# Optimization experiments

Measured on AMD Instinct MI355X. Metric: run time of the kernel, lower is better.

The kernel has to match this reference:

```python
import jax, jax.numpy as jnp
import numpy as np

NUM_GRAPHS = 1024
EPS = 1e-5  # BatchNorm eps
NEG_SLOPE = 0.2  # GATConv leaky_relu slope


def _bn(x, g, b):
    # train-mode BatchNorm over node/graph axis (biased variance, as torch)
    mu = jnp.mean(x, axis=0)
    var = jnp.mean((x - mu) ** 2, axis=0)
    return (x - mu) * jax.lax.rsqrt(var + EPS) * g + b


def _prelu(x, a):
    return jnp.where(x > 0, x, a * x)


def _gat_layer(x, src, dst, W, a_src, a_dst, bias, n_nodes):
    # single-head GATConv (heads=1, concat=True), self-loops already in src/dst
    h = x @ W                                            # [N, C]
    e = jax.nn.leaky_relu(jnp.take(h @ a_src, src) + jnp.take(h @ a_dst, dst), NEG_SLOPE)  # [E]
    m = jax.ops.segment_max(e, dst, num_segments=n_nodes)
    ex = jnp.exp(e - jnp.take(m, dst))
    denom = jax.ops.segment_sum(ex, dst, num_segments=n_nodes)
    alpha = ex / (jnp.take(denom, dst) + 1e-16)          # softmax over in-edges of each target
    out = jax.ops.segment_sum(jnp.take(h, src, axis=0) * alpha[:, None], dst, num_segments=n_nodes)
    return out + bias


def setup_inputs() -> dict:
    key = jax.random.key(0)
    ks = jax.random.split(key, 16)
    N, E, F, H, C = 500_000, 8_000_000, 7, 8, 2

    def gl(k, shp, fan_in):
        return (jax.random.normal(k, shp, jnp.float32) / np.sqrt(fan_in)).astype(jnp.float32)

    return {
        "x": jax.random.normal(ks[0], (N, F), jnp.float32),
        "edge_index": jax.random.randint(ks[1], (2, E), 0, N, jnp.int32),
        "batch": jnp.sort(jax.random.randint(ks[2], (N,), 0, NUM_GRAPHS, jnp.int32)),
        "W1": gl(ks[3], (F, H), F), "as1": gl(ks[4], (H,), H), "ad1": gl(ks[5], (H,), H), "b1": jnp.zeros((H,), jnp.float32),
        "W2": gl(ks[6], (H, H), H), "as2": gl(ks[7], (H,), H), "ad2": gl(ks[8], (H,), H), "b2": jnp.zeros((H,), jnp.float32),
        "W3": gl(ks[9], (H, H), H), "as3": gl(ks[10], (H,), H), "ad3": gl(ks[11], (H,), H), "b3": jnp.zeros((H,), jnp.float32),
        "g1": jnp.ones((H,), jnp.float32), "be1": jnp.zeros((H,), jnp.float32),
        "g2": jnp.ones((H,), jnp.float32), "be2": jnp.zeros((H,), jnp.float32),
        "g3": jnp.ones((H,), jnp.float32), "be3": jnp.zeros((H,), jnp.float32),
        "a_gnn": jnp.float32(0.25),
        "Wjk": gl(ks[12], (3 * H, H), 3 * H), "bjk": jnp.zeros((H,), jnp.float32),
        "Wm1": gl(ks[13], (H, H), H), "bm1": jnp.zeros((H,), jnp.float32),
        "gm": jnp.ones((H,), jnp.float32), "bem": jnp.zeros((H,), jnp.float32),
        "a_mlp": jnp.float32(0.25),
        "Wm2": gl(ks[14], (H, C), H), "bm2": jnp.zeros((C,), jnp.float32),
    }


def reference(x, edge_index, batch,
              W1, as1, ad1, b1, W2, as2, ad2, b2, W3, as3, ad3, b3,
              g1, be1, g2, be2, g3, be3, a_gnn, Wjk, bjk,
              Wm1, bm1, gm, bem, a_mlp, Wm2, bm2):
    N = x.shape[0]
    loop = jnp.arange(N, dtype=edge_index.dtype)  # GATConv add_self_loops=True
    src = jnp.concatenate([edge_index[0], loop])
    dst = jnp.concatenate([edge_index[1], loop])
    # 3-layer GAT, each: conv -> BatchNorm -> PReLU (dropout omitted: eval)
    h1 = _prelu(_bn(_gat_layer(x, src, dst, W1, as1, ad1, b1, N), g1, be1), a_gnn)
    h2 = _prelu(_bn(_gat_layer(h1, src, dst, W2, as2, ad2, b2, N), g2, be2), a_gnn)
    h3 = _prelu(_bn(_gat_layer(h2, src, dst, W3, as3, ad3, b3, N), g3, be3), a_gnn)
    # JumpingKnowledge 'cat' + projection to out_channels
    h = jnp.concatenate([h1, h2, h3], axis=1) @ Wjk + bjk   # [N, 8]
    pooled = jax.ops.segment_sum(h, batch, num_segments=NUM_GRAPHS)  # global_add_pool [G, 8]
    m1 = _prelu(_bn(pooled @ Wm1 + bm1, gm, bem), a_mlp)    # MLP hidden
    return m1 @ Wm2 + bm2                                    # [G, 2] logits
```

## Files before the change

kernel.cpp:

```cpp
#include <hip/hip_runtime.h>

typedef unsigned short u16;
typedef unsigned int   u32;

#define EPSBN     1e-5f
#define NEG_SLOPE 0.2f
#define NGRAPH    1024
#define NPB       512
#define CHUNK     16384
#define BKCAP     11264
#define NTILE     8
#define SLOTS     1536


static __device__ __forceinline__ float bfl(const u16* __restrict__ p, int i){
    return __uint_as_float(((u32)p[i]) << 16);
}
static __device__ __forceinline__ float ldf(const void* __restrict__ p, int i, bool f32){
    return f32 ? ((const float*)p)[i] : bfl((const u16*)p, i);
}
static __device__ __forceinline__ u16 f2bf(float f){
    u32 u = __float_as_uint(f);
    return (u16)((u + 0x7fffu + ((u >> 16) & 1u)) >> 16);
}
static __device__ __forceinline__ void unpack8(uint4 pk, float* a){
    a[0] = __uint_as_float((pk.x & 0xffffu) << 16);
    a[1] = __uint_as_float( pk.x & 0xffff0000u);
    a[2] = __uint_as_float((pk.y & 0xffffu) << 16);
    a[3] = __uint_as_float( pk.y & 0xffff0000u);
    a[4] = __uint_as_float((pk.z & 0xffffu) << 16);
    a[5] = __uint_as_float( pk.z & 0xffff0000u);
    a[6] = __uint_as_float((pk.w & 0xffffu) << 16);
    a[7] = __uint_as_float( pk.w & 0xffff0000u);
}
static __device__ __forceinline__ uint4 pack8(const float* a){
    uint4 pk;
    pk.x = (u32)f2bf(a[0]) | ((u32)f2bf(a[1])<<16);
    pk.y = (u32)f2bf(a[2]) | ((u32)f2bf(a[3])<<16);
    pk.z = (u32)f2bf(a[4]) | ((u32)f2bf(a[5])<<16);
    pk.w = (u32)f2bf(a[6]) | ((u32)f2bf(a[7])<<16);
    return pk;
}

static __device__ __forceinline__ int wave_scan_incl(int x){
    int lane = threadIdx.x & 63;
    #pragma unroll
    for (int off = 1; off < 64; off <<= 1){
        int y = __shfl_up(x, off, 64);
        if (lane >= off) x += y;
    }
    return x;
}
static __device__ __forceinline__ int block_scan_incl(int x, int* wpart){
    int t = threadIdx.x, lane = t & 63, wv = t >> 6;
    int nw = blockDim.x >> 6;
    int ws = wave_scan_incl(x);
    __syncthreads();
    if (lane == 63) wpart[wv] = ws;
    __syncthreads();
    if (wv == 0){
        int p = (lane < nw) ? wpart[lane] : 0;
        p = wave_scan_incl(p);
        if (lane < nw) wpart[lane] = p;
    }
    __syncthreads();
    int base = wv ? wpart[wv-1] : 0;
    return base + ws;
}

__global__ __launch_bounds__(1024) void k_binsort(const int* __restrict__ src,
                                                  const int* __restrict__ dst,
                                                  u32* __restrict__ stage,
                                                  int* __restrict__ matL,
                                                  int E, int B,
                                                  const u16* __restrict__ x16,
                                                  int* __restrict__ dflag,
                                                  float* __restrict__ statsAll){
    __shared__ u32 pr[CHUNK];
    __shared__ int h[2048];
    __shared__ int wpart[16];
    int c = blockIdx.x, t = threadIdx.x;
    if (c == 0){
        if (t < 64){
            bool hit = false;
            for (int i = t; i < 128; i += 64){
                float v = bfl(x16, i);
                if (!(fabsf(v) <= 1e6f)) hit = true;
            }
            unsigned long long m = __ballot(hit);
            if (t == 0) dflag[0] = (m != 0ull) ? 1 : 0;
        }
        if (t >= 64 && t < 112) statsAll[t - 64] = 0.f;
    }
    int e0 = c << 14, e1 = min(e0 + CHUNK, E), cn = e1 - e0;
    for (int b = t; b < B; b += 1024) h[b] = 0;
    __syncthreads();
    for (int i = e0 + t; i < e1; i += 1024) atomicAdd(&h[dst[i] >> 9], 1);
    __syncthreads();
    int base = t << 1, run = 0, loc[2];
    #pragma unroll
    for (int j = 0; j < 2; j++){
        int b = base + j;
        int v = (b < B) ? h[b] : 0;
        loc[j] = run; run += v;
    }
    int incl = block_scan_incl(run, wpart);
    int bex = incl - run;
    __syncthreads();
    #pragma unroll
    for (int j = 0; j < 2; j++){
        int b = base + j;
        if (b < B) h[b] = bex + loc[j];
    }
    __syncthreads();
    int* mrow = matL + (size_t)c * (B+1);
    for (int b = t; b < B; b += 1024) mrow[b] = h[b];
    if (t == 0) mrow[B] = cn;
    __syncthreads();
    for (int i = e0 + t; i < e1; i += 1024){
        int d = dst[i];
        int b = d >> 9;
        int p = atomicAdd(&h[b], 1);
        pr[p] = ((u32)src[i] << 9) | (u32)(d & 511);
    }
    __syncthreads();
    u32* srow = stage + ((size_t)c << 14);
    for (int i = t; i < cn; i += 1024) srow[i] = pr[i];
}

__global__ __launch_bounds__(1024) void k_bucket(const u32* __restrict__ stage,
                                                 const int* __restrict__ matL,
                                                 int* __restrict__ tileOfs,
                                                 u32* __restrict__ csr,
                                                 int N, int B, int NC){
    __shared__ u32 pr[BKCAP];
    __shared__ int hist[4096];
    __shared__ int sc[1024];
    __shared__ int lofsA[512];
    __shared__ int wpart[16];
    int k = blockIdx.x, t = threadIdx.x;
    int n0 = k << 9, n1 = min(n0 + NPB, N), nn = n1 - n0;
    int cnt = 0, lofs = 0;
    if (t < NC){
        lofs = matL[(size_t)t*(B+1) + k];
        cnt  = matL[(size_t)t*(B+1) + k + 1] - lofs;
    }
    if (t < 512) lofsA[t] = lofs;
    int incl1 = block_scan_incl(cnt, wpart);
    sc[t] = incl1;
    __syncthreads();
    int total = sc[1023];
    int ec    = min(total, BKCAP - nn);
    for (int pidx = t; pidx < ec; pidx += 1024){
        int lo = 0, hi = 511;
        while (lo < hi){ int mid = (lo + hi) >> 1; if (sc[mid] > pidx) hi = mid; else lo = mid + 1; }
        int segStart = lo ? sc[lo-1] : 0;
        pr[pidx] = stage[((size_t)lo << 14) + lofsA[lo] + (pidx - segStart)];
    }
    __syncthreads();
    for (int j = t; j < nn; j += 1024) pr[ec + j] = ((u32)(n0 + j) << 9) | (u32)j;
    int ecnt = ec + nn;
    for (int i = t; i < 4096; i += 1024) hist[i] = 0;
    __syncthreads();
    for (int i = t; i < ecnt; i += 1024){
        u32 pk = pr[i];
        int dl = pk & 511;
        int tile = min((int)(pk >> 9) >> 16, NTILE-1);
        atomicAdd(&hist[(tile << 9) + dl], 1);
    }
    __syncthreads();
    int base = t << 2, run = 0, loc[4];
    #pragma unroll
    for (int j = 0; j < 4; j++){ loc[j] = run; run += hist[base + j]; }
    int incl2 = block_scan_incl(run, wpart);
    int bex = incl2 - run;
    __syncthreads();
    #pragma unroll
    for (int j = 0; j < 4; j++) hist[base + j] = bex + loc[j];
    if ((t & 127) == 0) tileOfs[(size_t)k*9 + (t >> 7)] = bex;
    if (t == 0)         tileOfs[(size_t)k*9 + 8] = ecnt;
    __syncthreads();
    size_t wbase = (size_t)k * BKCAP;
    for (int i = t; i < ecnt; i += 1024){
        u32 pk = pr[i];
        int dl = pk & 511;
        int tile = min((int)(pk >> 9) >> 16, NTILE-1);
        int p = atomicAdd(&hist[(tile << 9) + dl], 1);
        csr[wbase + p] = pk;
    }
}

__global__ void k_transform(const uint4* __restrict__ actpk, const void* __restrict__ xraw,
                            const int* __restrict__ dflag, int fin,
                            const void* __restrict__ W, const void* __restrict__ adst,
                            const float* __restrict__ stats, const void* __restrict__ gamma,
                            const void* __restrict__ beta, const void* __restrict__ alpha,
                            uint4* __restrict__ hrec, float* __restrict__ hd, int n){
    const bool f32 = dflag[0] != 0;
    __shared__ float Wl[64], dl[8], scl[8], sft[8], alv;
    int t = threadIdx.x;
    if (t < 64)            Wl[t]   = (t < fin*8) ? ldf(W, t, f32) : 0.f;
    if (t >= 64 && t < 72) dl[t-64] = ldf(adst, t-64, f32);
    if (t == 80) alv = ldf(alpha, 0, f32);
    if (stats && t < 8){
        float invN = 1.f/(float)n;
        float mu  = stats[t]*invN;
        float var = fmaxf(stats[8+t]*invN - mu*mu, 0.f);
        float s   = ldf(gamma, t, f32)*rsqrtf(var + EPSBN);
        scl[t] = s; sft[t] = ldf(beta, t, f32) - mu*s;
    }
    __syncthreads();
    int i = blockIdx.x*blockDim.x + t;
    if (i >= n) return;
    float a[8];
    if (xraw){
        #pragma unroll
        for (int k=0;k<7;k++) a[k] = ldf(xraw, i*7 + k, f32);
        a[7] = 0.f;
    } else {
        unpack8(actpk[i], a);
        #pragma unroll
        for (int j=0;j<8;j++){
            float y = a[j]*scl[j] + sft[j];
            a[j] = (y > 0.f) ? y : alv*y;
        }
    }
    float h[8];
    #pragma unroll
    for (int j=0;j<8;j++){
        float acc = 0.f;
        #pragma unroll
        for (int k=0;k<8;k++) acc += a[k]*Wl[k*8+j];
        h[j] = acc;
    }
    float s2 = 0.f;
    #pragma unroll
    for (int j=0;j<8;j++) s2 += h[j]*dl[j];
    hd[i] = s2;
    hrec[i] = pack8(h);
}

__global__ __launch_bounds__(512) void k_aggregate(
        const u32* __restrict__ csr,
        const int* __restrict__ tileOfs,
        const uint4* __restrict__ hrec, const float* __restrict__ hd,
        const void* __restrict__ asrc, const int* __restrict__ dflag,
        uint4* __restrict__ act, float* __restrict__ stats, int n){
    const bool f32 = dflag[0] != 0;
    __shared__ u32   stg[4*SLOTS];
    __shared__ float swp[SLOTS];
    __shared__ u16   sdl[SLOTS];
    __shared__ float hdl[512];
    __shared__ u16 bs[512], be[512];
    __shared__ float alS[8];
    __shared__ float sred[8][16];
    __shared__ int tofS[9];
    int k = blockIdx.x, t = threadIdx.x;
    int n0 = k << 9;
    int nn = min(NPB, n - n0);
    if (t < 8) alS[t] = ldf(asrc, t, f32);
    if (t < 9) tofS[t] = tileOfs[(size_t)k*9 + t];
    hdl[t] = (t < nn) ? hd[n0 + t] : 0.f;
    const u32* ecsr = csr + (size_t)k * BKCAP;
    __syncthreads();
    float al[8];
    #pragma unroll
    for (int j = 0; j < 8; j++) al[j] = alS[j];
    float acc[8] = {0,0,0,0,0,0,0,0};
    float den = 0.f;

    int wt = 0, wc = 0;
    while (wt < NTILE && wc >= tofS[wt+1]){ wt++; if (wt < NTILE) wc = tofS[wt]; }

    u32 pkc[3]; uint4 hvc[3];
    if (wt < NTILE){
        int L = min(SLOTS, tofS[wt+1] - wc);
        #pragma unroll
        for (int j = 0; j < 3; j++) pkc[j] = ecsr[wc + min(t + (j << 9), L - 1)];
        #pragma unroll
        for (int j = 0; j < 3; j++) hvc[j] = hrec[pkc[j] >> 9];
    }

    while (wt < NTILE){
        int L = min(SLOTS, tofS[wt+1] - wc);
        __syncthreads();
        #pragma unroll
        for (int j = 0; j < 3; j++){
            int i = t + (j << 9);
            float h[8]; unpack8(hvc[j], h);
            int dl = (int)(pkc[j] & 511u);
            float e = hdl[dl];
            #pragma unroll
            for (int q = 0; q < 8; q++) e += h[q]*al[q];
            e = (e > 0.f) ? e : NEG_SLOPE*e;
            float w = __expf(e);
            if (i < L){
                stg[0*SLOTS + i] = hvc[j].x;
                stg[1*SLOTS + i] = hvc[j].y;
                stg[2*SLOTS + i] = hvc[j].z;
                stg[3*SLOTS + i] = hvc[j].w;
                swp[i] = w;
                sdl[i] = (u16)dl;
            }
        }
        bs[t] = 0; be[t] = 0;
        __syncthreads();
        int nwt = wt, nwc = wc + SLOTS;
        while (nwt < NTILE && nwc >= tofS[nwt+1]){ nwt++; if (nwt < NTILE) nwc = tofS[nwt]; }
        if (nwt < NTILE){
            int Ln = min(SLOTS, tofS[nwt+1] - nwc);
            #pragma unroll
            for (int j = 0; j < 3; j++) pkc[j] = ecsr[nwc + min(t + (j << 9), Ln - 1)];
            #pragma unroll
            for (int j = 0; j < 3; j++) hvc[j] = hrec[pkc[j] >> 9];
        }
        for (int i = t; i < L; i += 512){
            int dl = (int)sdl[i];
            if (i == 0){
                bs[dl] = 0;
            } else {
                int dp = (int)sdl[i - 1];
                if (dp != dl){ bs[dl] = (u16)i; be[dp] = (u16)i; }
            }
            if (i == L-1) be[dl] = (u16)L;
        }
        __syncthreads();
        {
            int p0 = bs[t], p1 = be[t];
            for (int p = p0; p < p1; ++p){
                uint4 hv = make_uint4(stg[0*SLOTS + p], stg[1*SLOTS + p],
                                      stg[2*SLOTS + p], stg[3*SLOTS + p]);
                float h[8]; unpack8(hv, h);
                float w = swp[p];
                den += w;
                #pragma unroll
                for (int q = 0; q < 8; q++) acc[q] += w*h[q];
            }
        }
        wt = nwt; wc = nwc;
    }

    float o[8] = {0,0,0,0,0,0,0,0};
    if (t < nn){
        float inv = 1.f/(den + 1e-16f);
        #pragma unroll
        for (int j = 0; j < 8; j++) o[j] = acc[j]*inv;
        act[n0 + t] = pack8(o);
    }
    float v[16];
    #pragma unroll
    for (int j=0;j<8;j++){ v[j]=o[j]; v[8+j]=o[j]*o[j]; }
    #pragma unroll
    for (int off=32; off>0; off>>=1){
        #pragma unroll
        for (int j=0;j<16;j++) v[j] += __shfl_down(v[j], off, 64);
    }
    int lane = t & 63, wv = t >> 6;
    if (lane == 0){
        #pragma unroll
        for (int j=0;j<16;j++) sred[wv][j] = v[j];
    }
    __syncthreads();
    if (t < 16){
        float tot = 0.f;
        #pragma unroll
        for (int w=0; w<8; w++) tot += sred[w][t];
        atomicAdd(&stats[t], tot);
    }
}

static __device__ __forceinline__ int lowerb(const int* __restrict__ a, int n, int key){
    int lo = 0, hi = n;
    while (lo < hi){ int mid = (lo + hi) >> 1; if (a[mid] < key) lo = mid + 1; else hi = mid; }
    return lo;
}

__global__ __launch_bounds__(256) void k_jkpool(
        const uint4* __restrict__ a1, const uint4* __restrict__ a2, const uint4* __restrict__ a3,
        const float* __restrict__ st1, const float* __restrict__ st2, const float* __restrict__ st3,
        const void* __restrict__ g1, const void* __restrict__ be1,
        const void* __restrict__ g2, const void* __restrict__ be2,
        const void* __restrict__ g3, const void* __restrict__ be3,
        const void* __restrict__ alpha,
        const void* __restrict__ Wjk, const void* __restrict__ bjk,
        const int* __restrict__ dflag,
        const int* __restrict__ batch, float* __restrict__ pooled, int n){
    const bool f32 = dflag[0] != 0;
    __shared__ float Wl[192], bl[8], scl[24], sft[24], alv;
    __shared__ int rng[2];
    int t = threadIdx.x, g = blockIdx.x;
    if (t < 192) Wl[t] = ldf(Wjk, t, f32);
    if (t < 8)   bl[t] = ldf(bjk, t, f32);
    if (t < 24){
        int L = t >> 3, j = t & 7;
        const float* st = (L==0)? st1 : (L==1)? st2 : st3;
        const void* gg  = (L==0)? g1  : (L==1)? g2  : g3;
        const void* bb_ = (L==0)? be1 : (L==1)? be2 : be3;
        float invN = 1.f/(float)n;
        float mu  = st[j]*invN;
        float var = fmaxf(st[8+j]*invN - mu*mu, 0.f);
        float s   = ldf(gg, j, f32)*rsqrtf(var + EPSBN);
        scl[t] = s; sft[t] = ldf(bb_, j, f32) - mu*s;
    }
    if (t == 30) alv = ldf(alpha, 0, f32);
    if (t == 0) rng[0] = lowerb(batch, n, g);
    if (t == 1) rng[1] = lowerb(batch, n, g+1);
    __syncthreads();
    int lo = rng[0], hi = rng[1];
    float pa[8] = {0,0,0,0,0,0,0,0};
    for (int i = lo + t; i < hi; i += 256){
        float c[24];
        unpack8(a1[i], c);
        unpack8(a2[i], c+8);
        unpack8(a3[i], c+16);
        #pragma unroll
        for (int k=0;k<24;k++){
            float y = c[k]*scl[k] + sft[k];
            c[k] = (y > 0.f) ? y : alv*y;
        }
        #pragma unroll
        for (int j=0;j<8;j++){
            float acc = bl[j];
            #pragma unroll
            for (int k=0;k<24;k++) acc += c[k]*Wl[k*8+j];
            pa[j] += acc;
        }
    }
    #pragma unroll
    for (int off=32; off>0; off>>=1){
        #pragma unroll
        for (int j=0;j<8;j++) pa[j] += __shfl_down(pa[j], off, 64);
    }
    __shared__ float sr[4][8];
    int lane = t & 63, wv = t >> 6;
    if (lane == 0){
        #pragma unroll
        for (int j=0;j<8;j++) sr[wv][j] = pa[j];
    }
    __syncthreads();
    if (t < 8){
        float tot = sr[0][t]+sr[1][t]+sr[2][t]+sr[3][t];
        pooled[(size_t)g*8 + t] = tot;
    }
}

__global__ __launch_bounds__(1024) void k_final(
        const float* __restrict__ pooled,
        const void* __restrict__ Wm1, const void* __restrict__ bm1,
        const void* __restrict__ gm, const void* __restrict__ bem,
        const void* __restrict__ am,
        const void* __restrict__ Wm2, const void* __restrict__ bm2,
        const int* __restrict__ dflag,
        float* __restrict__ out, int G){
    const bool f32 = dflag[0] != 0;
    int t = threadIdx.x;
    float tv[8] = {0,0,0,0,0,0,0,0};
    if (t < G){
        float r[8];
        #pragma unroll
        for (int j=0;j<8;j++) r[j] = pooled[(size_t)t*8+j];
        #pragma unroll
        for (int j=0;j<8;j++){
            float acc = ldf(bm1, j, f32);
            #pragma unroll
            for (int k=0;k<8;k++) acc += r[k]*ldf(Wm1, k*8+j, f32);
            tv[j] = acc;
        }
    }
    float v[16];
    #pragma unroll
    for (int j=0;j<8;j++){ v[j]=tv[j]; v[8+j]=tv[j]*tv[j]; }
    #pragma unroll
    for (int off=32; off>0; off>>=1){
        #pragma unroll
        for (int j=0;j<16;j++) v[j] += __shfl_down(v[j], off, 64);
    }
    __shared__ float sred[16][16];
    int lane = t & 63, wv = t >> 6;
    if (lane == 0){
        #pragma unroll
        for (int j=0;j<16;j++) sred[wv][j] = v[j];
    }
    __syncthreads();
    __shared__ float stt[16];
    if (t < 16){
        float tot = 0.f;
        #pragma unroll
        for (int w=0; w<16; w++) tot += sred[w][t];
        stt[t] = tot;
    }
    __syncthreads();
    if (t < G){
        float a = ldf(am, 0, f32);
        float invG = 1.f/(float)G;
        float m1[8];
        #pragma unroll
        for (int j=0;j<8;j++){
            float mu  = stt[j]*invG;
            float var = fmaxf(stt[8+j]*invG - mu*mu, 0.f);
            float y = (tv[j]-mu)*rsqrtf(var+EPSBN)*ldf(gm,j,f32)+ldf(bem,j,f32);
            m1[j] = (y>0.f)? y : a*y;
        }
        #pragma unroll
        for (int c=0;c<2;c++){
            float oacc = ldf(bm2, c, f32);
            #pragma unroll
            for (int k=0;k<8;k++) oacc += m1[k]*ldf(Wm2, k*2+c, f32);
            out[(size_t)t*2+c] = oacc;
        }
    }
}

extern "C" void kernel_launch(void* const* d_in, const int* in_sizes, int n_in,
                              void* d_out, int out_size, void* d_ws, size_t ws_size,
                              hipStream_t stream){
    const u16* x16   = (const u16*)d_in[0];
    const void* x    = d_in[0];
    const int* ei    = (const int*)d_in[1];
    const int* batch = (const int*)d_in[2];
    int N = in_sizes[2];
    int E = in_sizes[1] / 2;
    const int* srcA = ei;
    const int* dstA = ei + E;
    const void *W1=d_in[3],  *as1=d_in[4],  *ad1=d_in[5];
    const void *W2=d_in[7],  *as2=d_in[8],  *ad2=d_in[9];
    const void *W3=d_in[11], *as3=d_in[12], *ad3=d_in[13];
    const void *g1=d_in[15], *be1=d_in[16];
    const void *g2=d_in[17], *be2=d_in[18];
    const void *g3=d_in[19], *be3=d_in[20];
    const void *agnn=d_in[21];
    const void *Wjk=d_in[22], *bjk=d_in[23];
    const void *Wm1=d_in[24], *bm1=d_in[25];
    const void *gm =d_in[26], *bem=d_in[27];
    const void *amlp=d_in[28];
    const void *Wm2=d_in[29], *bm2=d_in[30];

    char* p = (char*)d_ws;
    auto carve = [&](size_t bytes) -> void* {
        void* r = (void*)p;
        p += (bytes + 255) & ~(size_t)255;
        return r;
    };
    int nb512 = (N + 511)/512;
    int B  = (N + NPB - 1) / NPB;
    int NC = (E + CHUNK - 1) / CHUNK;
    int*   dflag  = (int*)  carve(256);
    int*   tileOfs= (int*)  carve((size_t)B*9*4);
    int*   matL   = (int*)  carve((size_t)NC*(B+1)*4);
    u32*   stage  = (u32*)  carve((size_t)NC*CHUNK*4);
    u32*   csr    = (u32*)  carve((size_t)B*BKCAP*4);
    uint4* hrec   = (uint4*)carve((size_t)N*16);
    float* hd     = (float*)carve((size_t)N*4);
    uint4* act1   = (uint4*)carve((size_t)N*16);
    uint4* act2   = (uint4*)carve((size_t)N*16);
    uint4* act3   = (uint4*)carve((size_t)N*16);
    float* statsA = (float*)carve(256);
    float* stats1 = statsA;
    float* stats2 = statsA + 16;
    float* stats3 = statsA + 32;
    float* pooled = (float*)carve((size_t)NGRAPH*32);
    (void)ws_size; (void)n_in;

    k_binsort <<<NC, 1024, 0, stream>>>(srcA, dstA, stage, matL, E, B, x16, dflag, statsA);
    k_bucket  <<<B, 1024, 0, stream>>>(stage, matL, tileOfs, csr, N, B, NC);

    k_transform <<<nb512, 512, 0, stream>>>(nullptr, x, dflag, 7, W1, ad1,
                                            nullptr, nullptr, nullptr, agnn, hrec, hd, N);
    k_aggregate <<<B, 512, 0, stream>>>(csr, tileOfs, hrec, hd, as1, dflag, act1, stats1, N);
    k_transform <<<nb512, 512, 0, stream>>>(act1, nullptr, dflag, 8, W2, ad2,
                                            stats1, g1, be1, agnn, hrec, hd, N);
    k_aggregate <<<B, 512, 0, stream>>>(csr, tileOfs, hrec, hd, as2, dflag, act2, stats2, N);
    k_transform <<<nb512, 512, 0, stream>>>(act2, nullptr, dflag, 8, W3, ad3,
                                            stats2, g2, be2, agnn, hrec, hd, N);
    k_aggregate <<<B, 512, 0, stream>>>(csr, tileOfs, hrec, hd, as3, dflag, act3, stats3, N);

    k_jkpool<<<NGRAPH, 256, 0, stream>>>(act1, act2, act3, stats1, stats2, stats3,
                                         g1, be1, g2, be2, g3, be3, agnn,
                                         Wjk, bjk, dflag, batch, pooled, N);
    int G = out_size / 2;
    k_final <<<1, 1024, 0, stream>>>(pooled, Wm1, bm1, gm, bem, amlp, Wm2, bm2, dflag, (float*)d_out, G);
}
```

Baseline: 514.0 us.

## Fuse layer-1 transform into bucket kernel and MLP head into pooling kernel

Moves the first GAT layer's linear transform (x@W1 and the dst attention score) into the tail of k_bucket, so one kernel launch and a pass over x are removed. It also folds the final MLP/BatchNorm head into k_jkpool, using an atomic ticket so the last block to finish computes the output, which removes the separate single-block k_final launch. The cost is extra register and shared-memory pressure in k_bucket, plus a threadfence/atomic at the end of each jkpool block.

Measured after the change: 574.3 us. 1.12x slower.

```diff
diff --git a/kernel.cpp b/kernel.cpp
--- a/kernel.cpp
+++ b/kernel.cpp
@@ -88,7 +88,7 @@
                 if (!(fabsf(v) <= 1e6f)) hit = true;
             }
             unsigned long long m = __ballot(hit);
-            if (t == 0) dflag[0] = (m != 0ull) ? 1 : 0;
+            if (t == 0){ dflag[0] = (m != 0ull) ? 1 : 0; dflag[1] = 0; }
         }
         if (t >= 64 && t < 112) statsAll[t - 64] = 0.f;
     }
@@ -132,20 +132,30 @@
                                                  const int* __restrict__ matL,
                                                  int* __restrict__ tileOfs,
                                                  u32* __restrict__ csr,
-                                                 int N, int B, int NC){
+                                                 int N, int B, int NC,
+                                                 const void* __restrict__ x,
+                                                 const void* __restrict__ W1,
+                                                 const void* __restrict__ ad1,
+                                                 const int* __restrict__ dflag,
+                                                 uint4* __restrict__ hrec,
+                                                 float* __restrict__ hd){
     __shared__ u32 pr[BKCAP];
     __shared__ int hist[4096];
     __shared__ int sc[1024];
     __shared__ int lofsA[512];
     __shared__ int wpart[16];
+    __shared__ float WlT[64], adT[8];
     int k = blockIdx.x, t = threadIdx.x;
     int n0 = k << 9, n1 = min(n0 + NPB, N), nn = n1 - n0;
+    const bool f32 = dflag[0] != 0;
     int cnt = 0, lofs = 0;
     if (t < NC){
         lofs = matL[(size_t)t*(B+1) + k];
         cnt  = matL[(size_t)t*(B+1) + k + 1] - lofs;
     }
     if (t < 512) lofsA[t] = lofs;
+    if (t >= 512 && t < 576) WlT[t-512] = ((t-512) < 56) ? ldf(W1, t-512, f32) : 0.f;
+    if (t >= 576 && t < 584) adT[t-576] = ldf(ad1, t-576, f32);
     int incl1 = block_scan_incl(cnt, wpart);
     sc[t] = incl1;
     __syncthreads();
@@ -187,6 +197,26 @@
         int tile = min((int)(pk >> 9) >> 16, NTILE-1);
         int p = atomicAdd(&hist[(tile << 9) + dl], 1);
         csr[wbase + p] = pk;
+    }
+    if (t < nn){
+        int i = n0 + t;
+        float a[8];
+        #pragma unroll
+        for (int kk = 0; kk < 7; kk++) a[kk] = ldf(x, i*7 + kk, f32);
+        a[7] = 0.f;
+        float h[8];
+        #pragma unroll
+        for (int j = 0; j < 8; j++){
+            float acc = 0.f;
+            #pragma unroll
+            for (int kk = 0; kk < 8; kk++) acc += a[kk]*WlT[kk*8+j];
+            h[j] = acc;
+        }
+        float s2 = 0.f;
+        #pragma unroll
+        for (int j = 0; j < 8; j++) s2 += h[j]*adT[j];
+        hd[i] = s2;
+        hrec[i] = pack8(h);
     }
 }
 
@@ -384,7 +414,13 @@
         const void* __restrict__ alpha,
         const void* __restrict__ Wjk, const void* __restrict__ bjk,
         const int* __restrict__ dflag,
-        const int* __restrict__ batch, float* __restrict__ pooled, int n){
+        const int* __restrict__ batch, float* __restrict__ pooled, int n,
+        int* __restrict__ ticket,
+        const void* __restrict__ Wm1, const void* __restrict__ bm1,
+        const void* __restrict__ gm, const void* __restrict__ bem,
+        const void* __restrict__ am,
+        const void* __restrict__ Wm2, const void* __restrict__ bm2,
+        float* __restrict__ out, int G){
     const bool f32 = dflag[0] != 0;
     __shared__ float Wl[192], bl[8], scl[24], sft[24], alv;
     __shared__ int rng[2];
@@ -442,71 +478,77 @@
         float tot = sr[0][t]+sr[1][t]+sr[2][t]+sr[3][t];
         pooled[(size_t)g*8 + t] = tot;
     }
-}
-
-__global__ __launch_bounds__(1024) void k_final(
-        const float* __restrict__ pooled,
-        const void* __restrict__ Wm1, const void* __restrict__ bm1,
-        const void* __restrict__ gm, const void* __restrict__ bem,
-        const void* __restrict__ am,
-        const void* __restrict__ Wm2, const void* __restrict__ bm2,
-        const int* __restrict__ dflag,
-        float* __restrict__ out, int G){
-    const bool f32 = dflag[0] != 0;
-    int t = threadIdx.x;
-    float tv[8] = {0,0,0,0,0,0,0,0};
-    if (t < G){
-        float r[8];
-        #pragma unroll
-        for (int j=0;j<8;j++) r[j] = pooled[(size_t)t*8+j];
-        #pragma unroll
-        for (int j=0;j<8;j++){
-            float acc = ldf(bm1, j, f32);
-            #pragma unroll
-            for (int k=0;k<8;k++) acc += r[k]*ldf(Wm1, k*8+j, f32);
-            tv[j] = acc;
-        }
-    }
+    __threadfence();
+    __shared__ int isLast;
+    if (t == 0){
+        int my = atomicAdd(ticket, 1);
+        isLast = (my == (int)gridDim.x - 1) ? 1 : 0;
+    }
+    __syncthreads();
+    if (!isLast) return;
+    __threadfence();
+    float tv[4][8];
     float v[16];
     #pragma unroll
-    for (int j=0;j<8;j++){ v[j]=tv[j]; v[8+j]=tv[j]*tv[j]; }
+    for (int j=0;j<16;j++) v[j] = 0.f;
+    #pragma unroll
+    for (int gg=0; gg<4; gg++){
+        int g2 = t + (gg << 8);
+        #pragma unroll
+        for (int j=0;j<8;j++) tv[gg][j] = 0.f;
+        if (g2 < G){
+            float r[8];
+            #pragma unroll
+            for (int j=0;j<8;j++) r[j] = pooled[(size_t)g2*8+j];
+            #pragma unroll
+            for (int j=0;j<8;j++){
+                float acc = ldf(bm1, j, f32);
+                #pragma unroll
+                for (int kk=0;kk<8;kk++) acc += r[kk]*ldf(Wm1, kk*8+j, f32);
+                tv[gg][j] = acc;
+                v[j]   += acc;
+                v[8+j] += acc*acc;
+            }
+        }
+    }
     #pragma unroll
     for (int off=32; off>0; off>>=1){
         #pragma unroll
         for (int j=0;j<16;j++) v[j] += __shfl_down(v[j], off, 64);
     }
-    __shared__ float sred[16][16];
-    int lane = t & 63, wv = t >> 6;
+    __shared__ float sfin[4][16];
     if (lane == 0){
         #pragma unroll
-        for (int j=0;j<16;j++) sred[wv][j] = v[j];
+        for (int j=0;j<16;j++) sfin[wv][j] = v[j];
     }
     __syncthreads();
     __shared__ float stt[16];
     if (t < 16){
-        float tot = 0.f;
-        #pragma unroll
-        for (int w=0; w<16; w++) tot += sred[w][t];
+        float tot = sfin[0][t]+sfin[1][t]+sfin[2][t]+sfin[3][t];
         stt[t] = tot;
     }
     __syncthreads();
-    if (t < G){
-        float a = ldf(am, 0, f32);
-        float invG = 1.f/(float)G;
-        float m1[8];
-        #pragma unroll
-        for (int j=0;j<8;j++){
-            float mu  = stt[j]*invG;
-            float var = fmaxf(stt[8+j]*invG - mu*mu, 0.f);
-            float y = (tv[j]-mu)*rsqrtf(var+EPSBN)*ldf(gm,j,f32)+ldf(bem,j,f32);
-            m1[j] = (y>0.f)? y : a*y;
-        }
-        #pragma unroll
-        for (int c=0;c<2;c++){
-            float oacc = ldf(bm2, c, f32);
-            #pragma unroll
-            for (int k=0;k<8;k++) oacc += m1[k]*ldf(Wm2, k*2+c, f32);
-            out[(size_t)t*2+c] = oacc;
+    float a = ldf(am, 0, f32);
+    float invG = 1.f/(float)G;
+    #pragma unroll
+    for (int gg=0; gg<4; gg++){
+        int g2 = t + (gg << 8);
+        if (g2 < G){
+            float m1[8];
+            #pragma unroll
+            for (int j=0;j<8;j++){
+                float mu  = stt[j]*invG;
+                float var = fmaxf(stt[8+j]*invG - mu*mu, 0.f);
+                float y = (tv[gg][j]-mu)*rsqrtf(var+EPSBN)*ldf(gm,j,f32)+ldf(bem,j,f32);
+                m1[j] = (y>0.f)? y : a*y;
+            }
+            #pragma unroll
+            for (int c=0;c<2;c++){
+                float oacc = ldf(bm2, c, f32);
+                #pragma unroll
+                for (int kk=0;kk<8;kk++) oacc += m1[kk]*ldf(Wm2, kk*2+c, f32);
+                out[(size_t)g2*2+c] = oacc;
+            }
         }
     }
 }
@@ -562,10 +604,9 @@
     (void)ws_size; (void)n_in;
 
     k_binsort <<<NC, 1024, 0, stream>>>(srcA, dstA, stage, matL, E, B, x16, dflag, statsA);
-    k_bucket  <<<B, 1024, 0, stream>>>(stage, matL, tileOfs, csr, N, B, NC);
-
-    k_transform <<<nb512, 512, 0, stream>>>(nullptr, x, dflag, 7, W1, ad1,
-                                            nullptr, nullptr, nullptr, agnn, hrec, hd, N);
+    k_bucket  <<<B, 1024, 0, stream>>>(stage, matL, tileOfs, csr, N, B, NC,
+                                       x, W1, ad1, dflag, hrec, hd);
+
     k_aggregate <<<B, 512, 0, stream>>>(csr, tileOfs, hrec, hd, as1, dflag, act1, stats1, N);
     k_transform <<<nb512, 512, 0, stream>>>(act1, nullptr, dflag, 8, W2, ad2,
                                             stats1, g1, be1, agnn, hrec, hd, N);
@@ -574,9 +615,10 @@
                                             stats2, g2, be2, agnn, hrec, hd, N);
     k_aggregate <<<B, 512, 0, stream>>>(csr, tileOfs, hrec, hd, as3, dflag, act3, stats3, N);
 
+    int G = out_size / 2;
     k_jkpool<<<NGRAPH, 256, 0, stream>>>(act1, act2, act3, stats1, stats2, stats3,
                                          g1, be1, g2, be2, g3, be3, agnn,
-                                         Wjk, bjk, dflag, batch, pooled, N);
-    int G = out_size / 2;
-    k_final <<<1, 1024, 0, stream>>>(pooled, Wm1, bm1, gm, bem, amlp, Wm2, bm2, dflag, (float*)d_out, G);
-}
+                                         Wjk, bjk, dflag, batch, pooled, N,
+                                         dflag + 1, Wm1, bm1, gm, bem, amlp, Wm2, bm2,
+                                         (float*)d_out, G);
+}
```
